# Optimization experiments

Measured on AMD Instinct MI355X. Metric: run time of the kernel, lower is better.

Reference implementation:

```python
import jax, jax.numpy as jnp
import numpy as np

N_NODES = 50000


def gcn_layer(x, src, dst, W, b, norm):
    # x: [N, din]; src/dst: [E'] (self-loops included); norm: [E']
    h = x @ W                                # [N, dout]
    msg = h[src] * norm[:, None]             # [E', dout] gather + scale
    out = jax.ops.segment_sum(msg, dst, num_segments=x.shape[0])
    return out + b


def _with_self_loops_and_norm(edge_index, n):
    loop = jnp.arange(n, dtype=edge_index.dtype)
    src = jnp.concatenate([edge_index[0], loop])
    dst = jnp.concatenate([edge_index[1], loop])
    deg = jax.ops.segment_sum(jnp.ones_like(dst, dtype=jnp.float32), dst,
                              num_segments=n)
    dinv = jnp.where(deg > 0, jax.lax.rsqrt(jnp.maximum(deg, 1.0)), 0.0)
    norm = dinv[src] * dinv[dst]
    return src, dst, norm


def setup_inputs() -> dict:
    key = jax.random.key(0)
    ks = jax.random.split(key, 4)
    n, din, dh, dout = N_NODES, 128, 128, 64
    e_prev = jax.random.normal(ks[0], (n, din), dtype=jnp.float32)
    edge_index = jax.random.randint(ks[1], (2, 800000), 0, n, dtype=jnp.int64)
    W1 = jax.random.normal(ks[2], (din, dh), dtype=jnp.float32) / np.sqrt(din)
    b1 = jnp.zeros((dh,), dtype=jnp.float32)
    W2 = jax.random.normal(ks[3], (dh, dout), dtype=jnp.float32) / np.sqrt(dh)
    b2 = jnp.zeros((dout,), dtype=jnp.float32)
    return {"e_prev": e_prev, "edge_index": edge_index,
            "W1": W1, "b1": b1, "W2": W2, "b2": b2}


def reference(e_prev, edge_index, W1, b1, W2, b2):
    n = e_prev.shape[0]
    src, dst, norm = _with_self_loops_and_norm(edge_index, n)
    x = gcn_layer(e_prev, src, dst, W1, b1, norm)
    x = jax.nn.relu(x)
    x = gcn_layer(x, src, dst, W2, b2, norm)
    return x
```

## Files before the change

kernel.cpp:

```cpp
#include <hip/hip_runtime.h>
#include <hip/hip_fp16.h>


constexpr int DIN = 128;

__global__ void count_deg_k(const int* __restrict__ dst, int* __restrict__ cnt,
                            int* __restrict__ rank, int e2, int e) {
    int i = blockIdx.x * 256 + threadIdx.x;
    if (i >= e2) return;
    int2 d = reinterpret_cast<const int2*>(dst)[i];
    int r0 = atomicAdd(&cnt[d.x], 1);
    int r1 = (2 * i + 1 < e) ? atomicAdd(&cnt[d.y], 1) : 0;
    reinterpret_cast<int2*>(rank)[i] = make_int2(r0, r1);
}

__global__ __launch_bounds__(256) void scan1_k(const int* __restrict__ cnt,
                                               int* __restrict__ rowptr,
                                               int* __restrict__ bsum,
                                               float* __restrict__ dinv,
                                               int n_out, int n_cnt) {
    __shared__ int wsum[4];
    const int tid  = threadIdx.x;
    const int lane = tid & 63;
    const int wv   = tid >> 6;
    const int base = blockIdx.x * 1024 + tid * 4;

    int v0 = (base + 0 < n_cnt) ? cnt[base + 0] : 0;
    int v1 = (base + 1 < n_cnt) ? cnt[base + 1] : 0;
    int v2 = (base + 2 < n_cnt) ? cnt[base + 2] : 0;
    int v3 = (base + 3 < n_cnt) ? cnt[base + 3] : 0;
    int tsum = v0 + v1 + v2 + v3;

    if (base + 0 < n_cnt) dinv[base + 0] = rsqrtf((float)v0 + 1.0f);
    if (base + 1 < n_cnt) dinv[base + 1] = rsqrtf((float)v1 + 1.0f);
    if (base + 2 < n_cnt) dinv[base + 2] = rsqrtf((float)v2 + 1.0f);
    if (base + 3 < n_cnt) dinv[base + 3] = rsqrtf((float)v3 + 1.0f);

    int incl = tsum;
    for (int d = 1; d < 64; d <<= 1) {
        int t = __shfl_up(incl, d, 64);
        if (lane >= d) incl += t;
    }
    if (lane == 63) wsum[wv] = incl;
    __syncthreads();
    int woff = 0;
    for (int w = 0; w < wv; ++w) woff += wsum[w];
    int excl = woff + incl - tsum;

    int e0 = excl;
    int e1 = e0 + v0;
    int e2 = e1 + v1;
    int e3 = e2 + v2;
    if (base + 0 < n_out) rowptr[base + 0] = e0;
    if (base + 1 < n_out) rowptr[base + 1] = e1;
    if (base + 2 < n_out) rowptr[base + 2] = e2;
    if (base + 3 < n_out) rowptr[base + 3] = e3;

    if (tid == 255) bsum[blockIdx.x] = woff + incl;
}

__global__ __launch_bounds__(1024) void scan2_k(int* __restrict__ bsum, int nb) {
    __shared__ int sh[1024];
    const int t = threadIdx.x;
    int v = (t < nb) ? bsum[t] : 0;
    sh[t] = v;
    __syncthreads();
    for (int d = 1; d < 1024; d <<= 1) {
        int x = (t >= d) ? sh[t - d] : 0;
        __syncthreads();
        sh[t] += x;
        __syncthreads();
    }
    if (t < nb) bsum[t] = sh[t] - v;
}

__global__ void scan3_k(int* __restrict__ rowptr, const int* __restrict__ bsum, int n_out) {
    int i = blockIdx.x * 256 + threadIdx.x;
    if (i < n_out) rowptr[i] += bsum[i >> 10];
}

__global__ void fill_k(const int* __restrict__ src, const int* __restrict__ dst,
                       const int* __restrict__ rowptr, const int* __restrict__ rank,
                       int* __restrict__ col, int e2, int e) {
    int i = blockIdx.x * 256 + threadIdx.x;
    if (i >= e2) return;
    int2 d = reinterpret_cast<const int2*>(dst)[i];
    int2 r = reinterpret_cast<const int2*>(rank)[i];
    int2 s = reinterpret_cast<const int2*>(src)[i];
    col[rowptr[d.x] + r.x] = s.x;
    if (2 * i + 1 < e) col[rowptr[d.y] + r.y] = s.y;
}

template <typename TIN, int DOUT>
__global__ __launch_bounds__(256, 4) void gemm_scale_k(
    const TIN* __restrict__ X, const float* __restrict__ W,
    const float* __restrict__ dinv, __half* __restrict__ G, int N)
{
    constexpr int TM = 64;
    constexpr int C4 = DOUT / 4;
    constexpr int GROUPS = 256 / C4;
    constexpr int RPT = TM / GROUPS;

    __shared__ TIN sX[TM * DIN];

    const int tid  = threadIdx.x;
    const int base = blockIdx.x * TM;
    const float4* Wv = reinterpret_cast<const float4*>(W);

    constexpr int EPL = 16 / sizeof(TIN);
    for (int idx = tid; idx < TM * DIN / EPL; idx += 256) {
        int row  = idx / (DIN / EPL);
        int grow = base + row;
        uint4 v = make_uint4(0u, 0u, 0u, 0u);
        if (grow < N)
            v = reinterpret_cast<const uint4*>(X)[(size_t)grow * (DIN / EPL) + (idx % (DIN / EPL))];
        reinterpret_cast<uint4*>(sX)[idx] = v;
    }
    __syncthreads();

    const int cq = tid % C4;
    const int rg = tid / C4;

    float4 acc[RPT];
#pragma unroll
    for (int r = 0; r < RPT; ++r) acc[r] = make_float4(0.f, 0.f, 0.f, 0.f);

#pragma unroll 4
    for (int k = 0; k < DIN; ++k) {
        float4 w = Wv[k * C4 + cq];
#pragma unroll
        for (int r = 0; r < RPT; ++r) {
            float xv;
            if constexpr (sizeof(TIN) == 4) xv = ((const float*)sX)[(rg + r * GROUPS) * DIN + k];
            else                            xv = __half2float(((const __half*)sX)[(rg + r * GROUPS) * DIN + k]);
            acc[r].x = fmaf(xv, w.x, acc[r].x);
            acc[r].y = fmaf(xv, w.y, acc[r].y);
            acc[r].z = fmaf(xv, w.z, acc[r].z);
            acc[r].w = fmaf(xv, w.w, acc[r].w);
        }
    }

#pragma unroll
    for (int r = 0; r < RPT; ++r) {
        int row = base + rg + r * GROUPS;
        if (row < N) {
            float dv = dinv[row];
            __half2 p0 = __floats2half2_rn(acc[r].x * dv, acc[r].y * dv);
            __half2 p1 = __floats2half2_rn(acc[r].z * dv, acc[r].w * dv);
            uint2 packed = make_uint2(*reinterpret_cast<unsigned*>(&p0),
                                      *reinterpret_cast<unsigned*>(&p1));
            *reinterpret_cast<uint2*>(G + (size_t)row * DOUT + cq * 4) = packed;
        }
    }
}

template <int D, bool RELU, typename TOUT>
__global__ __launch_bounds__(256) void gather_k(
    const __half* __restrict__ G, const int* __restrict__ rowptr,
    const int* __restrict__ col, const float* __restrict__ dinv,
    const float* __restrict__ bias, TOUT* __restrict__ out, int N)
{
    constexpr int Q  = D / 8;
    constexpr int NS = 64 / Q;

    const int wave = (blockIdx.x * 256 + threadIdx.x) >> 6;
    const int lane = threadIdx.x & 63;
    if (wave >= N) return;
    const int node = wave;
    const int q    = lane % Q;
    const int slot = lane / Q;

    const uint4* G4 = reinterpret_cast<const uint4*>(G);

    float acc[8];
#pragma unroll
    for (int k = 0; k < 8; ++k) acc[k] = 0.f;

    auto accum = [&](uint4 raw) {
        const __half2* hp = reinterpret_cast<const __half2*>(&raw);
#pragma unroll
        for (int p = 0; p < 4; ++p) {
            float2 f = __half22float2(hp[p]);
            acc[2 * p]     += f.x;
            acc[2 * p + 1] += f.y;
        }
    };

    if (slot == 0) accum(G4[(size_t)node * Q + q]);
    const int beg = rowptr[node], end = rowptr[node + 1];
    int j = beg;

    for (; j + 4 * NS <= end; j += 4 * NS) {
        int s0 = col[j + 0 * NS + slot];
        int s1 = col[j + 1 * NS + slot];
        int s2 = col[j + 2 * NS + slot];
        int s3 = col[j + 3 * NS + slot];
        uint4 v0 = G4[(size_t)s0 * Q + q];
        uint4 v1 = G4[(size_t)s1 * Q + q];
        uint4 v2 = G4[(size_t)s2 * Q + q];
        uint4 v3 = G4[(size_t)s3 * Q + q];
        accum(v0); accum(v1); accum(v2); accum(v3);
    }
    for (; j + NS <= end; j += NS) {
        accum(G4[(size_t)col[j + slot] * Q + q]);
    }
    {
        int rem = end - j;
        if (slot < rem) accum(G4[(size_t)col[j + slot] * Q + q]);
    }

#pragma unroll
    for (int d = Q; d < 64; d <<= 1) {
#pragma unroll
        for (int k = 0; k < 8; ++k) acc[k] += __shfl_xor(acc[k], d, 64);
    }

    if (lane < Q) {
        float dv = dinv[node];
        const float4* bb = reinterpret_cast<const float4*>(bias + q * 8);
        float4 b0 = bb[0], b1 = bb[1];
        float o[8];
        o[0] = dv * acc[0] + b0.x;  o[1] = dv * acc[1] + b0.y;
        o[2] = dv * acc[2] + b0.z;  o[3] = dv * acc[3] + b0.w;
        o[4] = dv * acc[4] + b1.x;  o[5] = dv * acc[5] + b1.y;
        o[6] = dv * acc[6] + b1.z;  o[7] = dv * acc[7] + b1.w;
        if constexpr (RELU) {
#pragma unroll
            for (int k = 0; k < 8; ++k) o[k] = fmaxf(o[k], 0.f);
        }
        if constexpr (sizeof(TOUT) == 2) {
            __half2 h0 = __floats2half2_rn(o[0], o[1]);
            __half2 h1 = __floats2half2_rn(o[2], o[3]);
            __half2 h2 = __floats2half2_rn(o[4], o[5]);
            __half2 h3 = __floats2half2_rn(o[6], o[7]);
            uint4 packed = make_uint4(*reinterpret_cast<unsigned*>(&h0),
                                      *reinterpret_cast<unsigned*>(&h1),
                                      *reinterpret_cast<unsigned*>(&h2),
                                      *reinterpret_cast<unsigned*>(&h3));
            reinterpret_cast<uint4*>(out)[(size_t)node * Q + q] = packed;
        } else {
            float4* op = reinterpret_cast<float4*>((float*)out + (size_t)node * D + q * 8);
            op[0] = make_float4(o[0], o[1], o[2], o[3]);
            op[1] = make_float4(o[4], o[5], o[6], o[7]);
        }
    }
}

static inline size_t align256(size_t x) { return (x + 255) & ~size_t(255); }

extern "C" void kernel_launch(void* const* d_in, const int* in_sizes, int n_in,
                              void* d_out, int out_size, void* d_ws, size_t ws_size,
                              hipStream_t stream) {
    const float* e_prev = (const float*)d_in[0];
    const int*   eidx   = (const int*)d_in[1];
    const float* W1     = (const float*)d_in[2];
    const float* b1     = (const float*)d_in[3];
    const float* W2     = (const float*)d_in[4];
    const float* b2     = (const float*)d_in[5];

    const int dh   = in_sizes[3];
    const int din  = in_sizes[2] / dh;
    const int N    = in_sizes[0] / din;
    const int E    = in_sizes[1] / 2;
    (void)dh;

    const int* src = eidx;
    const int* dst = eidx + E;

    char* ws = (char*)d_ws;
    size_t off = 0;
    int*    cnt    = (int*)(ws + off);    off = align256(off + (size_t)N * 4);
    float*  dinv   = (float*)(ws + off);  off = align256(off + (size_t)N * 4);
    int*    rowptr = (int*)(ws + off);    off = align256(off + (size_t)(N + 1) * 4);
    int*    bsum   = (int*)(ws + off);    off = align256(off + (size_t)1024 * 4);
    int*    col    = (int*)(ws + off);    off = align256(off + (size_t)E * 4);
    int*    rank   = (int*)(ws + off);    off = align256(off + (size_t)E * 4);
    __half* gh     = (__half*)(ws + off); off = align256(off + (size_t)N * DIN * 2);
    __half* x2h    = (__half*)(ws + off); off = align256(off + (size_t)N * DIN * 2);
    (void)ws_size;

    float* outp = (float*)d_out;

    const int T = 256;
    const int gN = (N + T - 1) / T;
    const int E2 = (E + 1) / 2;
    const int gE2 = (E2 + T - 1) / T;
    const int gW = (N + 3) / 4;
    const int n_out = N + 1;
    const int nb = (n_out + 1023) / 1024;

    hipMemsetAsync(cnt, 0, (size_t)N * 4, stream);
    count_deg_k<<<gE2, T, 0, stream>>>(dst, cnt, rank, E2, E);
    scan1_k<<<nb, T, 0, stream>>>(cnt, rowptr, bsum, dinv, n_out, N);
    scan2_k<<<1, 1024, 0, stream>>>(bsum, nb);
    scan3_k<<<(n_out + T - 1) / T, T, 0, stream>>>(rowptr, bsum, n_out);
    fill_k<<<gE2, T, 0, stream>>>(src, dst, rowptr, rank, col, E2, E);

    gemm_scale_k<float, 128><<<(N + 63) / 64, T, 0, stream>>>(e_prev, W1, dinv, gh, N);
    gather_k<128, true, __half><<<gW, T, 0, stream>>>(gh, rowptr, col, dinv, b1, x2h, N);

    gemm_scale_k<__half, 64><<<(N + 63) / 64, T, 0, stream>>>(x2h, W2, dinv, gh, N);
    gather_k<64, false, float><<<gW, T, 0, stream>>>(gh, rowptr, col, dinv, b2, outp, N);
}
```

Before: 245.5 us.

## Split gather aggregation into feature-column chunks so each wave covers one chunk

New measurement: 311.1 us. 1.27x slower.

```diff
diff --git a/kernel.cpp b/kernel.cpp
--- a/kernel.cpp
+++ b/kernel.cpp
@@ -154,21 +154,25 @@
     }
 }
 
-template <int D, bool RELU, typename TOUT>
-__global__ __launch_bounds__(256) void gather_k(
+template <int D, int NCHUNK, bool RELU, typename TOUT>
+__global__ __launch_bounds__(256) void gather_chunk_k(
     const __half* __restrict__ G, const int* __restrict__ rowptr,
     const int* __restrict__ col, const float* __restrict__ dinv,
     const float* __restrict__ bias, TOUT* __restrict__ out, int N)
 {
-    constexpr int Q  = D / 8;
-    constexpr int NS = 64 / Q;
-
-    const int wave = (blockIdx.x * 256 + threadIdx.x) >> 6;
-    const int lane = threadIdx.x & 63;
-    if (wave >= N) return;
-    const int node = wave;
-    const int q    = lane % Q;
-    const int slot = lane / Q;
+    constexpr int CHUNK = D / NCHUNK;
+    constexpr int QL = CHUNK / 8;
+    constexpr int NS = 64 / QL;
+    constexpr int RS = D / 8;
+
+    const int gwave = (blockIdx.x * 256 + threadIdx.x) >> 6;
+    if (gwave >= N * NCHUNK) return;
+    const int chunk = gwave / N;
+    const int node  = gwave - chunk * N;
+    const int lane  = threadIdx.x & 63;
+    const int q     = lane % QL;
+    const int slot  = lane / QL;
+    const int cb    = chunk * QL;
 
     const uint4* G4 = reinterpret_cast<const uint4*>(G);
 
@@ -186,38 +190,31 @@
         }
     };
 
-    if (slot == 0) accum(G4[(size_t)node * Q + q]);
+    if (slot == 0) accum(G4[(size_t)node * RS + cb + q]);
     const int beg = rowptr[node], end = rowptr[node + 1];
+
     int j = beg;
-
-    for (; j + 4 * NS <= end; j += 4 * NS) {
-        int s0 = col[j + 0 * NS + slot];
-        int s1 = col[j + 1 * NS + slot];
-        int s2 = col[j + 2 * NS + slot];
-        int s3 = col[j + 3 * NS + slot];
-        uint4 v0 = G4[(size_t)s0 * Q + q];
-        uint4 v1 = G4[(size_t)s1 * Q + q];
-        uint4 v2 = G4[(size_t)s2 * Q + q];
-        uint4 v3 = G4[(size_t)s3 * Q + q];
-        accum(v0); accum(v1); accum(v2); accum(v3);
-    }
     for (; j + NS <= end; j += NS) {
-        accum(G4[(size_t)col[j + slot] * Q + q]);
+        int s = col[j + slot];
+        accum(G4[(size_t)s * RS + cb + q]);
     }
     {
         int rem = end - j;
-        if (slot < rem) accum(G4[(size_t)col[j + slot] * Q + q]);
-    }
-
-#pragma unroll
-    for (int d = Q; d < 64; d <<= 1) {
+        if (slot < rem) {
+            int s = col[j + slot];
+            accum(G4[(size_t)s * RS + cb + q]);
+        }
+    }
+
+#pragma unroll
+    for (int d = QL; d < 64; d <<= 1) {
 #pragma unroll
         for (int k = 0; k < 8; ++k) acc[k] += __shfl_xor(acc[k], d, 64);
     }
 
-    if (lane < Q) {
+    if (lane < QL) {
         float dv = dinv[node];
-        const float4* bb = reinterpret_cast<const float4*>(bias + q * 8);
+        const float4* bb = reinterpret_cast<const float4*>(bias + chunk * CHUNK + q * 8);
         float4 b0 = bb[0], b1 = bb[1];
         float o[8];
         o[0] = dv * acc[0] + b0.x;  o[1] = dv * acc[1] + b0.y;
@@ -237,9 +234,9 @@
                                       *reinterpret_cast<unsigned*>(&h1),
                                       *reinterpret_cast<unsigned*>(&h2),
                                       *reinterpret_cast<unsigned*>(&h3));
-            reinterpret_cast<uint4*>(out)[(size_t)node * Q + q] = packed;
+            reinterpret_cast<uint4*>((__half*)out + (size_t)node * D + chunk * CHUNK)[q] = packed;
         } else {
-            float4* op = reinterpret_cast<float4*>((float*)out + (size_t)node * D + q * 8);
+            float4* op = reinterpret_cast<float4*>((float*)out + (size_t)node * D + chunk * CHUNK + q * 8);
             op[0] = make_float4(o[0], o[1], o[2], o[3]);
             op[1] = make_float4(o[4], o[5], o[6], o[7]);
         }
@@ -282,10 +279,8 @@
     float* outp = (float*)d_out;
 
     const int T = 256;
-    const int gN = (N + T - 1) / T;
     const int E2 = (E + 1) / 2;
     const int gE2 = (E2 + T - 1) / T;
-    const int gW = (N + 3) / 4;
     const int n_out = N + 1;
     const int nb = (n_out + 1023) / 1024;
 
@@ -297,8 +292,16 @@
     fill_k<<<gE2, T, 0, stream>>>(src, dst, rowptr, rank, col, E2, E);
 
     gemm_scale_k<float, 128><<<(N + 63) / 64, T, 0, stream>>>(e_prev, W1, dinv, gh, N);
-    gather_k<128, true, __half><<<gW, T, 0, stream>>>(gh, rowptr, col, dinv, b1, x2h, N);
+    {
+        int waves = N * 4;
+        gather_chunk_k<128, 4, true, __half><<<(waves + 3) / 4, T, 0, stream>>>(
+            gh, rowptr, col, dinv, b1, x2h, N);
+    }
 
     gemm_scale_k<__half, 64><<<(N + 63) / 64, T, 0, stream>>>(x2h, W2, dinv, gh, N);
-    gather_k<64, false, float><<<gW, T, 0, stream>>>(gh, rowptr, col, dinv, b2, outp, N);
-}
+    {
+        int waves = N * 2;
+        gather_chunk_k<64, 2, false, float><<<(waves + 3) / 4, T, 0, stream>>>(
+            gh, rowptr, col, dinv, b2, outp, N);
+    }
+}
```
